# Kernel optimization log

Measured on AMD Instinct MI355X. Metric: run time of the kernel, lower is better.

The kernel has to match this reference:

```python
import jax, jax.numpy as jnp
import numpy as np

N = 1024    # num_points
HID = 1024  # Hamiltonian MLP hidden width


def setup_inputs() -> dict:
    key = jax.random.key(0)
    ks = jax.random.split(key, 6)
    def w(k, shape, fan_in):
        return jax.random.normal(k, shape, dtype=jnp.float32) / np.float32(np.sqrt(fan_in))
    return {
        "x": jax.random.normal(ks[0], (N,), dtype=jnp.float32),
        "q": jax.random.normal(ks[1], (N,), dtype=jnp.float32),
        "p": jax.random.normal(ks[2], (N,), dtype=jnp.float32),
        "W1": w(ks[3], (3 * N, HID), 3 * N),
        "b1": jnp.zeros((HID,), dtype=jnp.float32),
        "W2": w(ks[4], (HID, HID), HID),
        "b2": jnp.zeros((HID,), dtype=jnp.float32),
        "W3": w(ks[5], (HID, 1), HID),
        "b3": jnp.zeros((1,), dtype=jnp.float32),
    }


def _hamiltonian(z, W1, b1, W2, b2, W3, b3):
    # H: R^{3N} -> scalar (matches self.H(cat([x,q,p])).sum())
    h = jnp.tanh(z @ W1 + b1)
    h = jnp.tanh(h @ W2 + b2)
    return jnp.sum(h @ W3 + b3)


def reference(x, q, p, W1, b1, W2, b2, W3, b3):
    n = x.shape[0]

    def grads_qp(x_):
        # (dH/dq, dH/dp) as a function of x, with q,p closed over
        f = lambda q_, p_: _hamiltonian(jnp.concatenate([x_, q_, p_]), W1, b1, W2, b2, W3, b3)
        return jax.grad(f, argnums=(0, 1))(q, p)  # each [n]

    # Diagonal of cross-Hessian blocks via forward-over-reverse, batched over
    # all n basis directions at once (replaces the per-index autograd loop).
    eye = jnp.eye(n, dtype=x.dtype)

    def diag_entry(e_i, i):
        _, (dgq, dgp) = jax.jvp(grads_qp, (x,), (e_i,))
        return dgq[i], dgp[i]  # d2H/(dx_i dq_i), d2H/(dx_i dp_i)

    dH_dq_dx, dH_dp_dx = jax.vmap(diag_entry)(eye, jnp.arange(n))  # each [n]
    return dH_dp_dx, -dH_dq_dx
```

## Files before the change

### kernel.cpp

```cpp
#include <hip/hip_runtime.h>
#include <math.h>

typedef unsigned short u16;
typedef __bf16 bf16x8 __attribute__((ext_vector_type(8)));
typedef float f32x4 __attribute__((ext_vector_type(4)));

__device__ inline u16 bf16_rn(float x) {
    unsigned u = __float_as_uint(x);
    return (u16)((u + 0x7FFFu + ((u >> 16) & 1u)) >> 16);
}
__device__ inline uint2 pack4(u16 a, u16 b, u16 c, u16 d) {
    uint2 r;
    r.x = (unsigned)a | ((unsigned)b << 16);
    r.y = (unsigned)c | ((unsigned)d << 16);
    return r;
}
__device__ inline uint2 pack4f(float a, float b, float c, float d) {
    return pack4(bf16_rn(a), bf16_rn(b), bf16_rn(c), bf16_rn(d));
}
__device__ inline f32x4 mfma16(bf16x8 a, bf16x8 b, f32x4 c) {
    return __builtin_amdgcn_mfma_f32_16x16x32_bf16(a, b, c, 0, 0, 0);
}

__global__ __launch_bounds__(256) void k_pre(const float* __restrict__ x,
                                             const float* __restrict__ q,
                                             const float* __restrict__ p,
                                             const float* __restrict__ W1,
                                             u16* __restrict__ Ah,
                                             float* __restrict__ Upart,
                                             float* __restrict__ out,
                                             float* __restrict__ Vacc) {
    int b = blockIdx.x, t = threadIdx.x;
    if (b < 192) {
        int jc = b;
        int k = (jc & 3) * 256 + t;
        int j0 = (jc >> 2) * 64;
        __shared__ float zs[64];
        if (t < 64) {
            int j = j0 + t;
            zs[t] = (j < 1024) ? x[j] : (j < 2048 ? q[j - 1024] : p[j - 2048]);
        }
        __syncthreads();
        float acc = 0.f;
        if (j0 < 1024) {
#pragma unroll 8
            for (int j = 0; j < 64; ++j) {
                float v = W1[(j0 + j) * 1024 + k];
                Ah[(j0 + j) * 1024 + k] = bf16_rn(v);
                acc += zs[j] * v;
            }
        } else {
#pragma unroll 8
            for (int j = 0; j < 64; ++j) acc += zs[j] * W1[(j0 + j) * 1024 + k];
        }
        Upart[(jc >> 2) * 1024 + k] = acc;
    } else {
        int idx = ((b - 192) * 256 + t) * 4;
        if (idx < 2048) *(float4*)(out + idx) = make_float4(0.f, 0.f, 0.f, 0.f);
        else *(float4*)(Vacc + idx - 2048) = make_float4(0.f, 0.f, 0.f, 0.f);
    }
}

__global__ __launch_bounds__(256) void k_w2v(const float* __restrict__ W2,
                                             const float* __restrict__ b1,
                                             const float* __restrict__ Upart,
                                             float* __restrict__ H1g, float* __restrict__ D1g,
                                             u16* __restrict__ W2h,
                                             u16* __restrict__ WTh,
                                             float* __restrict__ Vacc) {
    __shared__ float T[64][65];
    __shared__ float hs[64], ds[64];
    __shared__ float red[4][64];
    int k0 = blockIdx.y * 64, m0 = blockIdx.x * 64;
    int t = threadIdx.x;
    {
        int lk = t & 63, g = t >> 6;
        float u = 0.f;
#pragma unroll
        for (int c = 0; c < 12; ++c) u += Upart[(g * 12 + c) * 1024 + k0 + lk];
        red[g][lk] = u;
    }
    __syncthreads();
    if (t < 64) {
        float u = red[0][t] + red[1][t] + red[2][t] + red[3][t];
        float h = tanhf(u + b1[k0 + t]);
        hs[t] = h;
        ds[t] = 1.f - h * h;
        if (m0 == 0) { H1g[k0 + t] = h; D1g[k0 + t] = 1.f - h * h; }
    }
    __syncthreads();
    int rr = t >> 4, cc = (t & 15) * 4;
    float4 vp = make_float4(0.f, 0.f, 0.f, 0.f);
#pragma unroll
    for (int j = 0; j < 4; ++j) {
        int r = rr + j * 16;
        float4 v = *(const float4*)(W2 + (k0 + r) * 1024 + m0 + cc);
        T[r][cc + 0] = v.x; T[r][cc + 1] = v.y; T[r][cc + 2] = v.z; T[r][cc + 3] = v.w;
        *(uint2*)&W2h[(k0 + r) * 1024 + m0 + cc] = pack4f(v.x, v.y, v.z, v.w);
        float hk = hs[r];
        vp.x += hk * v.x; vp.y += hk * v.y; vp.z += hk * v.z; vp.w += hk * v.w;
    }
    vp.x += __shfl_xor(vp.x, 16); vp.y += __shfl_xor(vp.y, 16);
    vp.z += __shfl_xor(vp.z, 16); vp.w += __shfl_xor(vp.w, 16);
    vp.x += __shfl_xor(vp.x, 32); vp.y += __shfl_xor(vp.y, 32);
    vp.z += __shfl_xor(vp.z, 32); vp.w += __shfl_xor(vp.w, 32);
    if (((t & 63) >> 4) == 0) {
        atomicAdd(&Vacc[m0 + cc + 0], vp.x);
        atomicAdd(&Vacc[m0 + cc + 1], vp.y);
        atomicAdd(&Vacc[m0 + cc + 2], vp.z);
        atomicAdd(&Vacc[m0 + cc + 3], vp.w);
    }
    __syncthreads();
#pragma unroll
    for (int j = 0; j < 4; ++j) {
        int mrow = rr + j * 16;
        float f0 = T[cc + 0][mrow] * ds[cc + 0];
        float f1 = T[cc + 1][mrow] * ds[cc + 1];
        float f2 = T[cc + 2][mrow] * ds[cc + 2];
        float f3 = T[cc + 3][mrow] * ds[cc + 3];
        *(uint2*)&WTh[(m0 + mrow) * 1024 + k0 + cc] = pack4f(f0, f1, f2, f3);
    }
}

#define LDK 68
__global__ __launch_bounds__(512) void k_gemm1(const u16* __restrict__ Ah,
                                               const u16* __restrict__ Bh,
                                               const float* __restrict__ Vacc,
                                               const float* __restrict__ b2,
                                               const float* __restrict__ W3,
                                               const float* __restrict__ W2,
                                               const float* __restrict__ H1,
                                               const float* __restrict__ D1,
                                               float* __restrict__ Avec,
                                               u16* __restrict__ Sh) {
    __shared__ u16 As[2][64 * LDK];
    __shared__ u16 Bs[2][64 * LDK];
    __shared__ float sv[1024];
    int tid = threadIdx.x;
    if (blockIdx.x == 16) {
        int kbase = blockIdx.y * 64;
#pragma unroll
        for (int j = 0; j < 2; ++j) {
            int m = tid + j * 512;
            float h = tanhf(Vacc[m] + b2[m]);
            sv[m] = (1.f - h * h) * W3[m];
        }
        __syncthreads();
        int g = tid >> 3, sub = tid & 7;
        int k = kbase + g;
        const float* wrow = W2 + k * 1024 + sub * 128;
        const float* svp = sv + sub * 128;
        float acc = 0.f;
#pragma unroll 8
        for (int j = 0; j < 128; ++j) acc += wrow[j] * svp[j];
        acc += __shfl_xor(acc, 1);
        acc += __shfl_xor(acc, 2);
        acc += __shfl_xor(acc, 4);
        if (sub == 0) Avec[k] = -2.f * H1[k] * D1[k] * acc;
        return;
    }
    int lane = tid & 63, wv = tid >> 6;
    int kh = wv >> 2, wy = (wv >> 1) & 1, wx = wv & 1;
    int i0 = blockIdx.y * 64, m0 = blockIdx.x * 64;
    int srow = tid >> 3, sseg = (tid & 7) * 8;
    int ldso = srow * LDK + sseg;
    const u16* ap = Ah + (i0 + srow) * 1024 + sseg;
    const u16* bp = Bh + (m0 + srow) * 1024 + sseg;
    int tx = lane & 15, qy = lane >> 4;
    int koff = kh * 32 + qy * 8;
    int raA[2], rbB[2];
    raA[0] = (wy * 32 + tx) * LDK + koff;
    raA[1] = raA[0] + 16 * LDK;
    rbB[0] = (wx * 32 + tx) * LDK + koff;
    rbB[1] = rbB[0] + 16 * LDK;
    f32x4 acc[2][2];
#pragma unroll
    for (int a = 0; a < 2; ++a)
#pragma unroll
        for (int b = 0; b < 2; ++b) acc[a][b] = (f32x4){0.f, 0.f, 0.f, 0.f};

    uint4 pa1 = *(const uint4*)(ap + 64);
    uint4 pc1 = *(const uint4*)(bp + 64);
    *(uint4*)&As[0][ldso] = *(const uint4*)(ap);
    *(uint4*)&Bs[0][ldso] = *(const uint4*)(bp);

    for (int k0 = 0; k0 < 1024; k0 += 64) {
        int buf = (k0 >> 6) & 1;
        int kn2 = (k0 + 128) & 1023;
        uint4 pa2 = *(const uint4*)(ap + kn2);
        uint4 pc2 = *(const uint4*)(bp + kn2);
        __syncthreads();
        bf16x8 aH0 = *(const bf16x8*)&As[buf][raA[0]];
        bf16x8 aH1 = *(const bf16x8*)&As[buf][raA[1]];
        bf16x8 bH0 = *(const bf16x8*)&Bs[buf][rbB[0]];
        bf16x8 bH1 = *(const bf16x8*)&Bs[buf][rbB[1]];
        acc[0][0] = mfma16(aH0, bH0, acc[0][0]);
        acc[0][1] = mfma16(aH0, bH1, acc[0][1]);
        acc[1][0] = mfma16(aH1, bH0, acc[1][0]);
        acc[1][1] = mfma16(aH1, bH1, acc[1][1]);
        int nb = buf ^ 1;
        *(uint4*)&As[nb][ldso] = pa1;
        *(uint4*)&Bs[nb][ldso] = pc1;
        pa1 = pa2; pc1 = pc2;
    }
    __syncthreads();
    f32x4* mrg = (f32x4*)&As[0][0];
    if (kh == 1) {
#pragma unroll
        for (int si = 0; si < 2; ++si)
#pragma unroll
            for (int sj = 0; sj < 2; ++sj)
                mrg[(((wy * 2 + wx) * 4 + si * 2 + sj) * 4 + qy) * 16 + tx] = acc[si][sj];
    }
    __syncthreads();
    if (kh == 0) {
#pragma unroll
        for (int si = 0; si < 2; ++si)
#pragma unroll
            for (int sj = 0; sj < 2; ++sj) {
                f32x4 o = mrg[(((wy * 2 + wx) * 4 + si * 2 + sj) * 4 + qy) * 16 + tx];
                acc[si][sj][0] += o[0]; acc[si][sj][1] += o[1];
                acc[si][sj][2] += o[2]; acc[si][sj][3] += o[3];
            }
#pragma unroll
        for (int sj = 0; sj < 2; ++sj) {
            int m = m0 + wx * 32 + sj * 16 + tx;
            float hv = tanhf(Vacc[m] + b2[m]);
            float d2 = 1.f - hv * hv;
            float cm = -2.f * hv * d2 * W3[m];
#pragma unroll
            for (int si = 0; si < 2; ++si) {
                int ib = i0 + wy * 32 + si * 16 + qy * 4;
#pragma unroll
                for (int r = 0; r < 4; ++r)
                    Sh[(ib + r) * 1024 + m] = bf16_rn(acc[si][sj][r] * cm);
            }
        }
    }
}

__global__ __launch_bounds__(512) void k_gemm2(const u16* __restrict__ Sh,
                                               const u16* __restrict__ W2h,
                                               const float* __restrict__ W1,
                                               const float* __restrict__ D1,
                                               const float* __restrict__ Avec,
                                               float* __restrict__ out) {
    __shared__ u16 As[2][64 * LDK];
    __shared__ u16 Bs[2][64 * LDK];
    int tid = threadIdx.x, lane = tid & 63, wv = tid >> 6;
    int kh = wv >> 2, wy = (wv >> 1) & 1, wx = wv & 1;
    int i0 = blockIdx.y * 64, k0g = blockIdx.x * 64;
    int srow = tid >> 3, sseg = (tid & 7) * 8;
    int ldso = srow * LDK + sseg;
    const u16* ap = Sh + (i0 + srow) * 1024 + sseg;
    const u16* bp = W2h + (k0g + srow) * 1024 + sseg;
    int tx = lane & 15, qy = lane >> 4;
    int koff = kh * 32 + qy * 8;
    int raA[2], rbB[2];
    raA[0] = (wy * 32 + tx) * LDK + koff;
    raA[1] = raA[0] + 16 * LDK;
    rbB[0] = (wx * 32 + tx) * LDK + koff;
    rbB[1] = rbB[0] + 16 * LDK;
    f32x4 acc[2][2];
#pragma unroll
    for (int a = 0; a < 2; ++a)
#pragma unroll
        for (int b = 0; b < 2; ++b) acc[a][b] = (f32x4){0.f, 0.f, 0.f, 0.f};

    uint4 pa1 = *(const uint4*)(ap + 64);
    uint4 pc1 = *(const uint4*)(bp + 64);
    *(uint4*)&As[0][ldso] = *(const uint4*)(ap);
    *(uint4*)&Bs[0][ldso] = *(const uint4*)(bp);

    for (int m0 = 0; m0 < 1024; m0 += 64) {
        int buf = (m0 >> 6) & 1;
        int mn2 = (m0 + 128) & 1023;
        uint4 pa2 = *(const uint4*)(ap + mn2);
        uint4 pc2 = *(const uint4*)(bp + mn2);
        __syncthreads();
        bf16x8 aH0 = *(const bf16x8*)&As[buf][raA[0]];
        bf16x8 aH1 = *(const bf16x8*)&As[buf][raA[1]];
        bf16x8 bH0 = *(const bf16x8*)&Bs[buf][rbB[0]];
        bf16x8 bH1 = *(const bf16x8*)&Bs[buf][rbB[1]];
        acc[0][0] = mfma16(aH0, bH0, acc[0][0]);
        acc[0][1] = mfma16(aH0, bH1, acc[0][1]);
        acc[1][0] = mfma16(aH1, bH0, acc[1][0]);
        acc[1][1] = mfma16(aH1, bH1, acc[1][1]);
        int nb = buf ^ 1;
        *(uint4*)&As[nb][ldso] = pa1;
        *(uint4*)&Bs[nb][ldso] = pc1;
        pa1 = pa2; pc1 = pc2;
    }
    __syncthreads();
    f32x4* mrg = (f32x4*)&As[0][0];
    if (kh == 1) {
#pragma unroll
        for (int si = 0; si < 2; ++si)
#pragma unroll
            for (int sj = 0; sj < 2; ++sj)
                mrg[(((wy * 2 + wx) * 4 + si * 2 + sj) * 4 + qy) * 16 + tx] = acc[si][sj];
    }
    __syncthreads();
    if (kh == 0) {
#pragma unroll
        for (int si = 0; si < 2; ++si)
#pragma unroll
            for (int sj = 0; sj < 2; ++sj) {
                f32x4 o = mrg[(((wy * 2 + wx) * 4 + si * 2 + sj) * 4 + qy) * 16 + tx];
                acc[si][sj][0] += o[0]; acc[si][sj][1] += o[1];
                acc[si][sj][2] += o[2]; acc[si][sj][3] += o[3];
            }
        int kk[2];
        float d1v[2], avv[2];
#pragma unroll
        for (int sj = 0; sj < 2; ++sj) {
            kk[sj] = k0g + wx * 32 + sj * 16 + tx;
            d1v[sj] = D1[kk[sj]];
            avv[sj] = Avec[kk[sj]];
        }
#pragma unroll
        for (int si = 0; si < 2; ++si) {
            int ib = i0 + wy * 32 + si * 16 + qy * 4;
#pragma unroll
            for (int r = 0; r < 4; ++r) {
                int i = ib + r;
                float pq = 0.f, pp = 0.f;
#pragma unroll
                for (int sj = 0; sj < 2; ++sj) {
                    int k = kk[sj];
                    float dr = avv[sj] * W1[i * 1024 + k] + d1v[sj] * acc[si][sj][r];
                    pq += W1[(1024 + i) * 1024 + k] * dr;
                    pp += W1[(2048 + i) * 1024 + k] * dr;
                }
                for (int o = 1; o < 16; o <<= 1) {
                    pq += __shfl_xor(pq, o);
                    pp += __shfl_xor(pp, o);
                }
                if (tx == 0) {
                    atomicAdd(&out[i], pp);
                    atomicAdd(&out[1024 + i], -pq);
                }
            }
        }
    }
}

extern "C" void kernel_launch(void* const* d_in, const int* in_sizes, int n_in,
                              void* d_out, int out_size, void* d_ws, size_t ws_size,
                              hipStream_t stream) {
    const float* x = (const float*)d_in[0];
    const float* q = (const float*)d_in[1];
    const float* p = (const float*)d_in[2];
    const float* W1 = (const float*)d_in[3];
    const float* b1 = (const float*)d_in[4];
    const float* W2 = (const float*)d_in[5];
    const float* b2 = (const float*)d_in[6];
    const float* W3 = (const float*)d_in[7];
    float* out = (float*)d_out;
    float* ws = (float*)d_ws;
    float* H1 = ws, *D1 = ws + 1024, *Avec = ws + 2048, *Vacc = ws + 3072;
    float* Upart = ws + 4096;
    u16* u0 = (u16*)(ws + 65536);
    u16* Ah = u0;
    u16* WTh = u0 + 1048576;
    u16* W2h = u0 + 2097152;
    u16* Sh = u0 + 3145728;

    k_pre<<<195, 256, 0, stream>>>(x, q, p, W1, Ah, Upart, out, Vacc);
    k_w2v<<<dim3(16, 16), 256, 0, stream>>>(W2, b1, Upart, H1, D1, W2h, WTh, Vacc);
    k_gemm1<<<dim3(17, 16), 512, 0, stream>>>(Ah, WTh, Vacc, b2, W3, W2, H1, D1, Avec, Sh);
    k_gemm2<<<dim3(16, 16), 512, 0, stream>>>(Sh, W2h, W1, D1, Avec, out);
}
```

Before: 119.2 us.

## Fuse four kernels into one cooperative kernel with grid-wide syncs

Replaces the four separate launches (pre, w2v, gemm1, gemm2) with a single cooperative kernel of 256 blocks that uses grid.sync between stages. The Avec matvec that used to run in an extra 17th column of gemm1 blocks is now spread across all blocks after their GEMM tile, and stage work is remapped onto 512-thread blocks. This aims to remove the launch gaps and tail effects between kernels, at the cost of grid-barrier overhead and some threads idling in the stages that only use 256 threads.

Result: slower. 235.0 us (+97.2%).

```diff
diff --git a/kernel.cpp b/kernel.cpp
--- a/kernel.cpp
+++ b/kernel.cpp
@@ -1,5 +1,8 @@
 #include <hip/hip_runtime.h>
+#include <hip/hip_cooperative_groups.h>
 #include <math.h>
+
+namespace cg = cooperative_groups;
 
 typedef unsigned short u16;
 typedef __bf16 bf16x8 __attribute__((ext_vector_type(8)));
@@ -22,123 +25,199 @@
     return __builtin_amdgcn_mfma_f32_16x16x32_bf16(a, b, c, 0, 0, 0);
 }
 
-__global__ __launch_bounds__(256) void k_pre(const float* __restrict__ x,
-                                             const float* __restrict__ q,
-                                             const float* __restrict__ p,
-                                             const float* __restrict__ W1,
-                                             u16* __restrict__ Ah,
-                                             float* __restrict__ Upart,
-                                             float* __restrict__ out,
-                                             float* __restrict__ Vacc) {
-    int b = blockIdx.x, t = threadIdx.x;
-    if (b < 192) {
-        int jc = b;
-        int k = (jc & 3) * 256 + t;
+#define LDK 68
+#define SMEM_BYTES 39040
+
+__global__ __launch_bounds__(512) void k_fused(
+    const float* __restrict__ x, const float* __restrict__ q, const float* __restrict__ p,
+    const float* __restrict__ W1, const float* __restrict__ b1,
+    const float* __restrict__ W2, const float* __restrict__ b2, const float* __restrict__ W3,
+    float* __restrict__ out,
+    float* __restrict__ H1, float* __restrict__ D1, float* __restrict__ Avec,
+    float* __restrict__ Vacc, float* __restrict__ Upart,
+    u16* __restrict__ Ah, u16* __restrict__ WTh, u16* __restrict__ W2h, u16* __restrict__ Sh) {
+    __shared__ __align__(16) char smem[SMEM_BYTES];
+    cg::grid_group grid = cg::this_grid();
+    int tid = threadIdx.x, bid = blockIdx.x;
+
+    if (bid < 96) {
+        float* zs2 = (float*)smem;
+        int half = tid >> 8, t2 = tid & 255;
+        int jc = bid * 2 + half;
+        int k = (jc & 3) * 256 + t2;
         int j0 = (jc >> 2) * 64;
-        __shared__ float zs[64];
-        if (t < 64) {
-            int j = j0 + t;
-            zs[t] = (j < 1024) ? x[j] : (j < 2048 ? q[j - 1024] : p[j - 2048]);
-        }
-        __syncthreads();
+        if (t2 < 64) {
+            int j = j0 + t2;
+            zs2[half * 64 + t2] = (j < 1024) ? x[j] : (j < 2048 ? q[j - 1024] : p[j - 2048]);
+        }
+        __syncthreads();
+        const float* zsl = zs2 + half * 64;
         float acc = 0.f;
         if (j0 < 1024) {
 #pragma unroll 8
             for (int j = 0; j < 64; ++j) {
                 float v = W1[(j0 + j) * 1024 + k];
                 Ah[(j0 + j) * 1024 + k] = bf16_rn(v);
-                acc += zs[j] * v;
+                acc += zsl[j] * v;
             }
         } else {
 #pragma unroll 8
-            for (int j = 0; j < 64; ++j) acc += zs[j] * W1[(j0 + j) * 1024 + k];
+            for (int j = 0; j < 64; ++j) acc += zsl[j] * W1[(j0 + j) * 1024 + k];
         }
         Upart[(jc >> 2) * 1024 + k] = acc;
-    } else {
-        int idx = ((b - 192) * 256 + t) * 4;
-        if (idx < 2048) *(float4*)(out + idx) = make_float4(0.f, 0.f, 0.f, 0.f);
-        else *(float4*)(Vacc + idx - 2048) = make_float4(0.f, 0.f, 0.f, 0.f);
+    } else if (bid == 96) {
+        for (int s = tid; s < 768; s += 512) {
+            int idx = s * 4;
+            if (idx < 2048) *(float4*)(out + idx) = make_float4(0.f, 0.f, 0.f, 0.f);
+            else *(float4*)(Vacc + idx - 2048) = make_float4(0.f, 0.f, 0.f, 0.f);
+        }
     }
-}
-
-__global__ __launch_bounds__(256) void k_w2v(const float* __restrict__ W2,
-                                             const float* __restrict__ b1,
-                                             const float* __restrict__ Upart,
-                                             float* __restrict__ H1g, float* __restrict__ D1g,
-                                             u16* __restrict__ W2h,
-                                             u16* __restrict__ WTh,
-                                             float* __restrict__ Vacc) {
-    __shared__ float T[64][65];
-    __shared__ float hs[64], ds[64];
-    __shared__ float red[4][64];
-    int k0 = blockIdx.y * 64, m0 = blockIdx.x * 64;
-    int t = threadIdx.x;
+    grid.sync();
+
     {
-        int lk = t & 63, g = t >> 6;
-        float u = 0.f;
-#pragma unroll
-        for (int c = 0; c < 12; ++c) u += Upart[(g * 12 + c) * 1024 + k0 + lk];
-        red[g][lk] = u;
+        float(*T)[65] = (float(*)[65])smem;
+        float* red = (float*)(smem + 16640);
+        float* hs = (float*)(smem + 18688);
+        float* ds = (float*)(smem + 18944);
+        int k0 = (bid >> 4) * 64, m0 = (bid & 15) * 64;
+        {
+            int g = tid >> 6, lk = tid & 63;
+            float u = 0.f;
+#pragma unroll
+            for (int c = 0; c < 6; ++c) u += Upart[(g * 6 + c) * 1024 + k0 + lk];
+            red[g * 64 + lk] = u;
+        }
+        __syncthreads();
+        if (tid < 64) {
+            float u = 0.f;
+#pragma unroll
+            for (int g = 0; g < 8; ++g) u += red[g * 64 + tid];
+            float h = tanhf(u + b1[k0 + tid]);
+            hs[tid] = h;
+            ds[tid] = 1.f - h * h;
+            if (m0 == 0) { H1[k0 + tid] = h; D1[k0 + tid] = 1.f - h * h; }
+        }
+        __syncthreads();
+        int t = tid;
+        int rr = (t & 255) >> 4, cc = (t & 15) * 4;
+        if (t < 256) {
+            float4 vp = make_float4(0.f, 0.f, 0.f, 0.f);
+#pragma unroll
+            for (int j = 0; j < 4; ++j) {
+                int r = rr + j * 16;
+                float4 v = *(const float4*)(W2 + (k0 + r) * 1024 + m0 + cc);
+                T[r][cc + 0] = v.x; T[r][cc + 1] = v.y; T[r][cc + 2] = v.z; T[r][cc + 3] = v.w;
+                *(uint2*)&W2h[(k0 + r) * 1024 + m0 + cc] = pack4f(v.x, v.y, v.z, v.w);
+                float hk = hs[r];
+                vp.x += hk * v.x; vp.y += hk * v.y; vp.z += hk * v.z; vp.w += hk * v.w;
+            }
+            vp.x += __shfl_xor(vp.x, 16); vp.y += __shfl_xor(vp.y, 16);
+            vp.z += __shfl_xor(vp.z, 16); vp.w += __shfl_xor(vp.w, 16);
+            vp.x += __shfl_xor(vp.x, 32); vp.y += __shfl_xor(vp.y, 32);
+            vp.z += __shfl_xor(vp.z, 32); vp.w += __shfl_xor(vp.w, 32);
+            if (((t & 63) >> 4) == 0) {
+                atomicAdd(&Vacc[m0 + cc + 0], vp.x);
+                atomicAdd(&Vacc[m0 + cc + 1], vp.y);
+                atomicAdd(&Vacc[m0 + cc + 2], vp.z);
+                atomicAdd(&Vacc[m0 + cc + 3], vp.w);
+            }
+        }
+        __syncthreads();
+        if (t < 256) {
+#pragma unroll
+            for (int j = 0; j < 4; ++j) {
+                int mrow = rr + j * 16;
+                float f0 = T[cc + 0][mrow] * ds[cc + 0];
+                float f1 = T[cc + 1][mrow] * ds[cc + 1];
+                float f2 = T[cc + 2][mrow] * ds[cc + 2];
+                float f3 = T[cc + 3][mrow] * ds[cc + 3];
+                *(uint2*)&WTh[(m0 + mrow) * 1024 + k0 + cc] = pack4f(f0, f1, f2, f3);
+            }
+        }
     }
-    __syncthreads();
-    if (t < 64) {
-        float u = red[0][t] + red[1][t] + red[2][t] + red[3][t];
-        float h = tanhf(u + b1[k0 + t]);
-        hs[t] = h;
-        ds[t] = 1.f - h * h;
-        if (m0 == 0) { H1g[k0 + t] = h; D1g[k0 + t] = 1.f - h * h; }
-    }
-    __syncthreads();
-    int rr = t >> 4, cc = (t & 15) * 4;
-    float4 vp = make_float4(0.f, 0.f, 0.f, 0.f);
-#pragma unroll
-    for (int j = 0; j < 4; ++j) {
-        int r = rr + j * 16;
-        float4 v = *(const float4*)(W2 + (k0 + r) * 1024 + m0 + cc);
-        T[r][cc + 0] = v.x; T[r][cc + 1] = v.y; T[r][cc + 2] = v.z; T[r][cc + 3] = v.w;
-        *(uint2*)&W2h[(k0 + r) * 1024 + m0 + cc] = pack4f(v.x, v.y, v.z, v.w);
-        float hk = hs[r];
-        vp.x += hk * v.x; vp.y += hk * v.y; vp.z += hk * v.z; vp.w += hk * v.w;
-    }
-    vp.x += __shfl_xor(vp.x, 16); vp.y += __shfl_xor(vp.y, 16);
-    vp.z += __shfl_xor(vp.z, 16); vp.w += __shfl_xor(vp.w, 16);
-    vp.x += __shfl_xor(vp.x, 32); vp.y += __shfl_xor(vp.y, 32);
-    vp.z += __shfl_xor(vp.z, 32); vp.w += __shfl_xor(vp.w, 32);
-    if (((t & 63) >> 4) == 0) {
-        atomicAdd(&Vacc[m0 + cc + 0], vp.x);
-        atomicAdd(&Vacc[m0 + cc + 1], vp.y);
-        atomicAdd(&Vacc[m0 + cc + 2], vp.z);
-        atomicAdd(&Vacc[m0 + cc + 3], vp.w);
-    }
-    __syncthreads();
-#pragma unroll
-    for (int j = 0; j < 4; ++j) {
-        int mrow = rr + j * 16;
-        float f0 = T[cc + 0][mrow] * ds[cc + 0];
-        float f1 = T[cc + 1][mrow] * ds[cc + 1];
-        float f2 = T[cc + 2][mrow] * ds[cc + 2];
-        float f3 = T[cc + 3][mrow] * ds[cc + 3];
-        *(uint2*)&WTh[(m0 + mrow) * 1024 + k0 + cc] = pack4f(f0, f1, f2, f3);
-    }
-}
-
-#define LDK 68
-__global__ __launch_bounds__(512) void k_gemm1(const u16* __restrict__ Ah,
-                                               const u16* __restrict__ Bh,
-                                               const float* __restrict__ Vacc,
-                                               const float* __restrict__ b2,
-                                               const float* __restrict__ W3,
-                                               const float* __restrict__ W2,
-                                               const float* __restrict__ H1,
-                                               const float* __restrict__ D1,
-                                               float* __restrict__ Avec,
-                                               u16* __restrict__ Sh) {
-    __shared__ u16 As[2][64 * LDK];
-    __shared__ u16 Bs[2][64 * LDK];
-    __shared__ float sv[1024];
-    int tid = threadIdx.x;
-    if (blockIdx.x == 16) {
-        int kbase = blockIdx.y * 64;
+    grid.sync();
+
+    {
+        u16* As = (u16*)smem;
+        u16* Bs = (u16*)(smem + 17408);
+        float* sv = (float*)(smem + 34816);
+        float* redA = (float*)(smem + 38912);
+        int lane = tid & 63, wv = tid >> 6;
+        int kh = wv >> 2, wy = (wv >> 1) & 1, wx = wv & 1;
+        int i0 = (bid >> 4) * 64, m0 = (bid & 15) * 64;
+        int srow = tid >> 3, sseg = (tid & 7) * 8;
+        int ldso = srow * LDK + sseg;
+        const u16* ap = Ah + (i0 + srow) * 1024 + sseg;
+        const u16* bp = WTh + (m0 + srow) * 1024 + sseg;
+        int tx = lane & 15, qy = lane >> 4;
+        int koff = kh * 32 + qy * 8;
+        int raA0 = (wy * 32 + tx) * LDK + koff, raA1 = raA0 + 16 * LDK;
+        int rbB0 = (wx * 32 + tx) * LDK + koff, rbB1 = rbB0 + 16 * LDK;
+        f32x4 acc[2][2];
+#pragma unroll
+        for (int a = 0; a < 2; ++a)
+#pragma unroll
+            for (int b = 0; b < 2; ++b) acc[a][b] = (f32x4){0.f, 0.f, 0.f, 0.f};
+
+        uint4 pa1 = *(const uint4*)(ap + 64);
+        uint4 pc1 = *(const uint4*)(bp + 64);
+        *(uint4*)&As[ldso] = *(const uint4*)(ap);
+        *(uint4*)&Bs[ldso] = *(const uint4*)(bp);
+
+        for (int k0 = 0; k0 < 1024; k0 += 64) {
+            int buf = ((k0 >> 6) & 1) * 4352;
+            int kn2 = (k0 + 128) & 1023;
+            uint4 pa2 = *(const uint4*)(ap + kn2);
+            uint4 pc2 = *(const uint4*)(bp + kn2);
+            __syncthreads();
+            bf16x8 aH0 = *(const bf16x8*)&As[buf + raA0];
+            bf16x8 aH1 = *(const bf16x8*)&As[buf + raA1];
+            bf16x8 bH0 = *(const bf16x8*)&Bs[buf + rbB0];
+            bf16x8 bH1 = *(const bf16x8*)&Bs[buf + rbB1];
+            acc[0][0] = mfma16(aH0, bH0, acc[0][0]);
+            acc[0][1] = mfma16(aH0, bH1, acc[0][1]);
+            acc[1][0] = mfma16(aH1, bH0, acc[1][0]);
+            acc[1][1] = mfma16(aH1, bH1, acc[1][1]);
+            int nb = buf ^ 4352;
+            *(uint4*)&As[nb + ldso] = pa1;
+            *(uint4*)&Bs[nb + ldso] = pc1;
+            pa1 = pa2; pc1 = pc2;
+        }
+        __syncthreads();
+        f32x4* mrg = (f32x4*)As;
+        if (kh == 1) {
+#pragma unroll
+            for (int si = 0; si < 2; ++si)
+#pragma unroll
+                for (int sj = 0; sj < 2; ++sj)
+                    mrg[(((wy * 2 + wx) * 4 + si * 2 + sj) * 4 + qy) * 16 + tx] = acc[si][sj];
+        }
+        __syncthreads();
+        if (kh == 0) {
+#pragma unroll
+            for (int si = 0; si < 2; ++si)
+#pragma unroll
+                for (int sj = 0; sj < 2; ++sj) {
+                    f32x4 o = mrg[(((wy * 2 + wx) * 4 + si * 2 + sj) * 4 + qy) * 16 + tx];
+                    acc[si][sj][0] += o[0]; acc[si][sj][1] += o[1];
+                    acc[si][sj][2] += o[2]; acc[si][sj][3] += o[3];
+                }
+#pragma unroll
+            for (int sj = 0; sj < 2; ++sj) {
+                int m = m0 + wx * 32 + sj * 16 + tx;
+                float hv = tanhf(Vacc[m] + b2[m]);
+                float d2 = 1.f - hv * hv;
+                float cm = -2.f * hv * d2 * W3[m];
+#pragma unroll
+                for (int si = 0; si < 2; ++si) {
+                    int ib = i0 + wy * 32 + si * 16 + qy * 4;
+#pragma unroll
+                    for (int r = 0; r < 4; ++r)
+                        Sh[(ib + r) * 1024 + m] = bf16_rn(acc[si][sj][r] * cm);
+                }
+            }
+        }
+        __syncthreads();
 #pragma unroll
         for (int j = 0; j < 2; ++j) {
             int m = tid + j * 512;
@@ -146,199 +225,119 @@
             sv[m] = (1.f - h * h) * W3[m];
         }
         __syncthreads();
-        int g = tid >> 3, sub = tid & 7;
-        int k = kbase + g;
-        const float* wrow = W2 + k * 1024 + sub * 128;
-        const float* svp = sv + sub * 128;
-        float acc = 0.f;
-#pragma unroll 8
-        for (int j = 0; j < 128; ++j) acc += wrow[j] * svp[j];
-        acc += __shfl_xor(acc, 1);
-        acc += __shfl_xor(acc, 2);
-        acc += __shfl_xor(acc, 4);
-        if (sub == 0) Avec[k] = -2.f * H1[k] * D1[k] * acc;
-        return;
+        {
+            int kA = bid * 4 + (wv >> 1);
+            int off = (wv & 1) * 512 + lane * 8;
+            const float* wr = W2 + kA * 1024 + off;
+            const float* svp = sv + off;
+            float a = 0.f;
+#pragma unroll
+            for (int j = 0; j < 8; ++j) a += wr[j] * svp[j];
+#pragma unroll
+            for (int o = 1; o < 64; o <<= 1) a += __shfl_xor(a, o);
+            if (lane == 0) redA[wv] = a;
+        }
+        __syncthreads();
+        if (tid < 4) {
+            int kA = bid * 4 + tid;
+            Avec[kA] = -2.f * H1[kA] * D1[kA] * (redA[tid * 2] + redA[tid * 2 + 1]);
+        }
     }
-    int lane = tid & 63, wv = tid >> 6;
-    int kh = wv >> 2, wy = (wv >> 1) & 1, wx = wv & 1;
-    int i0 = blockIdx.y * 64, m0 = blockIdx.x * 64;
-    int srow = tid >> 3, sseg = (tid & 7) * 8;
-    int ldso = srow * LDK + sseg;
-    const u16* ap = Ah + (i0 + srow) * 1024 + sseg;
-    const u16* bp = Bh + (m0 + srow) * 1024 + sseg;
-    int tx = lane & 15, qy = lane >> 4;
-    int koff = kh * 32 + qy * 8;
-    int raA[2], rbB[2];
-    raA[0] = (wy * 32 + tx) * LDK + koff;
-    raA[1] = raA[0] + 16 * LDK;
-    rbB[0] = (wx * 32 + tx) * LDK + koff;
-    rbB[1] = rbB[0] + 16 * LDK;
-    f32x4 acc[2][2];
-#pragma unroll
-    for (int a = 0; a < 2; ++a)
-#pragma unroll
-        for (int b = 0; b < 2; ++b) acc[a][b] = (f32x4){0.f, 0.f, 0.f, 0.f};
-
-    uint4 pa1 = *(const uint4*)(ap + 64);
-    uint4 pc1 = *(const uint4*)(bp + 64);
-    *(uint4*)&As[0][ldso] = *(const uint4*)(ap);
-    *(uint4*)&Bs[0][ldso] = *(const uint4*)(bp);
-
-    for (int k0 = 0; k0 < 1024; k0 += 64) {
-        int buf = (k0 >> 6) & 1;
-        int kn2 = (k0 + 128) & 1023;
-        uint4 pa2 = *(const uint4*)(ap + kn2);
-        uint4 pc2 = *(const uint4*)(bp + kn2);
-        __syncthreads();
-        bf16x8 aH0 = *(const bf16x8*)&As[buf][raA[0]];
-        bf16x8 aH1 = *(const bf16x8*)&As[buf][raA[1]];
-        bf16x8 bH0 = *(const bf16x8*)&Bs[buf][rbB[0]];
-        bf16x8 bH1 = *(const bf16x8*)&Bs[buf][rbB[1]];
-        acc[0][0] = mfma16(aH0, bH0, acc[0][0]);
-        acc[0][1] = mfma16(aH0, bH1, acc[0][1]);
-        acc[1][0] = mfma16(aH1, bH0, acc[1][0]);
-        acc[1][1] = mfma16(aH1, bH1, acc[1][1]);
-        int nb = buf ^ 1;
-        *(uint4*)&As[nb][ldso] = pa1;
-        *(uint4*)&Bs[nb][ldso] = pc1;
-        pa1 = pa2; pc1 = pc2;
-    }
-    __syncthreads();
-    f32x4* mrg = (f32x4*)&As[0][0];
-    if (kh == 1) {
-#pragma unroll
-        for (int si = 0; si < 2; ++si)
-#pragma unroll
-            for (int sj = 0; sj < 2; ++sj)
-                mrg[(((wy * 2 + wx) * 4 + si * 2 + sj) * 4 + qy) * 16 + tx] = acc[si][sj];
-    }
-    __syncthreads();
-    if (kh == 0) {
-#pragma unroll
-        for (int si = 0; si < 2; ++si)
+    grid.sync();
+
+    {
+        u16* As = (u16*)smem;
+        u16* Bs = (u16*)(smem + 17408);
+        int lane = tid & 63, wv = tid >> 6;
+        int kh = wv >> 2, wy = (wv >> 1) & 1, wx = wv & 1;
+        int i0 = (bid >> 4) * 64, k0g = (bid & 15) * 64;
+        int srow = tid >> 3, sseg = (tid & 7) * 8;
+        int ldso = srow * LDK + sseg;
+        const u16* ap = Sh + (i0 + srow) * 1024 + sseg;
+        const u16* bp = W2h + (k0g + srow) * 1024 + sseg;
+        int tx = lane & 15, qy = lane >> 4;
+        int koff = kh * 32 + qy * 8;
+        int raA0 = (wy * 32 + tx) * LDK + koff, raA1 = raA0 + 16 * LDK;
+        int rbB0 = (wx * 32 + tx) * LDK + koff, rbB1 = rbB0 + 16 * LDK;
+        f32x4 acc[2][2];
+#pragma unroll
+        for (int a = 0; a < 2; ++a)
+#pragma unroll
+            for (int b = 0; b < 2; ++b) acc[a][b] = (f32x4){0.f, 0.f, 0.f, 0.f};
+
+        uint4 pa1 = *(const uint4*)(ap + 64);
+        uint4 pc1 = *(const uint4*)(bp + 64);
+        *(uint4*)&As[ldso] = *(const uint4*)(ap);
+        *(uint4*)&Bs[ldso] = *(const uint4*)(bp);
+
+        for (int m0 = 0; m0 < 1024; m0 += 64) {
+            int buf = ((m0 >> 6) & 1) * 4352;
+            int mn2 = (m0 + 128) & 1023;
+            uint4 pa2 = *(const uint4*)(ap + mn2);
+            uint4 pc2 = *(const uint4*)(bp + mn2);
+            __syncthreads();
+            bf16x8 aH0 = *(const bf16x8*)&As[buf + raA0];
+            bf16x8 aH1 = *(const bf16x8*)&As[buf + raA1];
+            bf16x8 bH0 = *(const bf16x8*)&Bs[buf + rbB0];
+            bf16x8 bH1 = *(const bf16x8*)&Bs[buf + rbB1];
+            acc[0][0] = mfma16(aH0, bH0, acc[0][0]);
+            acc[0][1] = mfma16(aH0, bH1, acc[0][1]);
+            acc[1][0] = mfma16(aH1, bH0, acc[1][0]);
+            acc[1][1] = mfma16(aH1, bH1, acc[1][1]);
+            int nb = buf ^ 4352;
+            *(uint4*)&As[nb + ldso] = pa1;
+            *(uint4*)&Bs[nb + ldso] = pc1;
+            pa1 = pa2; pc1 = pc2;
+        }
+        __syncthreads();
+        f32x4* mrg = (f32x4*)As;
+        if (kh == 1) {
+#pragma unroll
+            for (int si = 0; si < 2; ++si)
+#pragma unroll
+                for (int sj = 0; sj < 2; ++sj)
+                    mrg[(((wy * 2 + wx) * 4 + si * 2 + sj) * 4 + qy) * 16 + tx] = acc[si][sj];
+        }
+        __syncthreads();
+        if (kh == 0) {
+#pragma unroll
+            for (int si = 0; si < 2; ++si)
+#pragma unroll
+                for (int sj = 0; sj < 2; ++sj) {
+                    f32x4 o = mrg[(((wy * 2 + wx) * 4 + si * 2 + sj) * 4 + qy) * 16 + tx];
+                    acc[si][sj][0] += o[0]; acc[si][sj][1] += o[1];
+                    acc[si][sj][2] += o[2]; acc[si][sj][3] += o[3];
+                }
+            int kk[2];
+            float d1v[2], avv[2];
 #pragma unroll
             for (int sj = 0; sj < 2; ++sj) {
-                f32x4 o = mrg[(((wy * 2 + wx) * 4 + si * 2 + sj) * 4 + qy) * 16 + tx];
-                acc[si][sj][0] += o[0]; acc[si][sj][1] += o[1];
-                acc[si][sj][2] += o[2]; acc[si][sj][3] += o[3];
-            }
-#pragma unroll
-        for (int sj = 0; sj < 2; ++sj) {
-            int m = m0 + wx * 32 + sj * 16 + tx;
-            float hv = tanhf(Vacc[m] + b2[m]);
-            float d2 = 1.f - hv * hv;
-            float cm = -2.f * hv * d2 * W3[m];
+                kk[sj] = k0g + wx * 32 + sj * 16 + tx;
+                d1v[sj] = D1[kk[sj]];
+                avv[sj] = Avec[kk[sj]];
+            }
 #pragma unroll
             for (int si = 0; si < 2; ++si) {
                 int ib = i0 + wy * 32 + si * 16 + qy * 4;
 #pragma unroll
-                for (int r = 0; r < 4; ++r)
-                    Sh[(ib + r) * 1024 + m] = bf16_rn(acc[si][sj][r] * cm);
-            }
-        }
-    }
-}
-
-__global__ __launch_bounds__(512) void k_gemm2(const u16* __restrict__ Sh,
-                                               const u16* __restrict__ W2h,
-                                               const float* __restrict__ W1,
-                                               const float* __restrict__ D1,
-                                               const float* __restrict__ Avec,
-                                               float* __restrict__ out) {
-    __shared__ u16 As[2][64 * LDK];
-    __shared__ u16 Bs[2][64 * LDK];
-    int tid = threadIdx.x, lane = tid & 63, wv = tid >> 6;
-    int kh = wv >> 2, wy = (wv >> 1) & 1, wx = wv & 1;
-    int i0 = blockIdx.y * 64, k0g = blockIdx.x * 64;
-    int srow = tid >> 3, sseg = (tid & 7) * 8;
-    int ldso = srow * LDK + sseg;
-    const u16* ap = Sh + (i0 + srow) * 1024 + sseg;
-    const u16* bp = W2h + (k0g + srow) * 1024 + sseg;
-    int tx = lane & 15, qy = lane >> 4;
-    int koff = kh * 32 + qy * 8;
-    int raA[2], rbB[2];
-    raA[0] = (wy * 32 + tx) * LDK + koff;
-    raA[1] = raA[0] + 16 * LDK;
-    rbB[0] = (wx * 32 + tx) * LDK + koff;
-    rbB[1] = rbB[0] + 16 * LDK;
-    f32x4 acc[2][2];
-#pragma unroll
-    for (int a = 0; a < 2; ++a)
-#pragma unroll
-        for (int b = 0; b < 2; ++b) acc[a][b] = (f32x4){0.f, 0.f, 0.f, 0.f};
-
-    uint4 pa1 = *(const uint4*)(ap + 64);
-    uint4 pc1 = *(const uint4*)(bp + 64);
-    *(uint4*)&As[0][ldso] = *(const uint4*)(ap);
-    *(uint4*)&Bs[0][ldso] = *(const uint4*)(bp);
-
-    for (int m0 = 0; m0 < 1024; m0 += 64) {
-        int buf = (m0 >> 6) & 1;
-        int mn2 = (m0 + 128) & 1023;
-        uint4 pa2 = *(const uint4*)(ap + mn2);
-        uint4 pc2 = *(const uint4*)(bp + mn2);
-        __syncthreads();
-        bf16x8 aH0 = *(const bf16x8*)&As[buf][raA[0]];
-        bf16x8 aH1 = *(const bf16x8*)&As[buf][raA[1]];
-        bf16x8 bH0 = *(const bf16x8*)&Bs[buf][rbB[0]];
-        bf16x8 bH1 = *(const bf16x8*)&Bs[buf][rbB[1]];
-        acc[0][0] = mfma16(aH0, bH0, acc[0][0]);
-        acc[0][1] = mfma16(aH0, bH1, acc[0][1]);
-        acc[1][0] = mfma16(aH1, bH0, acc[1][0]);
-        acc[1][1] = mfma16(aH1, bH1, acc[1][1]);
-        int nb = buf ^ 1;
-        *(uint4*)&As[nb][ldso] = pa1;
-        *(uint4*)&Bs[nb][ldso] = pc1;
-        pa1 = pa2; pc1 = pc2;
-    }
-    __syncthreads();
-    f32x4* mrg = (f32x4*)&As[0][0];
-    if (kh == 1) {
-#pragma unroll
-        for (int si = 0; si < 2; ++si)
-#pragma unroll
-            for (int sj = 0; sj < 2; ++sj)
-                mrg[(((wy * 2 + wx) * 4 + si * 2 + sj) * 4 + qy) * 16 + tx] = acc[si][sj];
-    }
-    __syncthreads();
-    if (kh == 0) {
-#pragma unroll
-        for (int si = 0; si < 2; ++si)
-#pragma unroll
-            for (int sj = 0; sj < 2; ++sj) {
-                f32x4 o = mrg[(((wy * 2 + wx) * 4 + si * 2 + sj) * 4 + qy) * 16 + tx];
-                acc[si][sj][0] += o[0]; acc[si][sj][1] += o[1];
-                acc[si][sj][2] += o[2]; acc[si][sj][3] += o[3];
-            }
-        int kk[2];
-        float d1v[2], avv[2];
-#pragma unroll
-        for (int sj = 0; sj < 2; ++sj) {
-            kk[sj] = k0g + wx * 32 + sj * 16 + tx;
-            d1v[sj] = D1[kk[sj]];
-            avv[sj] = Avec[kk[sj]];
-        }
-#pragma unroll
-        for (int si = 0; si < 2; ++si) {
-            int ib = i0 + wy * 32 + si * 16 + qy * 4;
-#pragma unroll
-            for (int r = 0; r < 4; ++r) {
-                int i = ib + r;
-                float pq = 0.f, pp = 0.f;
-#pragma unroll
-                for (int sj = 0; sj < 2; ++sj) {
-                    int k = kk[sj];
-                    float dr = avv[sj] * W1[i * 1024 + k] + d1v[sj] * acc[si][sj][r];
-                    pq += W1[(1024 + i) * 1024 + k] * dr;
-                    pp += W1[(2048 + i) * 1024 + k] * dr;
-                }
-                for (int o = 1; o < 16; o <<= 1) {
-                    pq += __shfl_xor(pq, o);
-                    pp += __shfl_xor(pp, o);
-                }
-                if (tx == 0) {
-                    atomicAdd(&out[i], pp);
-                    atomicAdd(&out[1024 + i], -pq);
+                for (int r = 0; r < 4; ++r) {
+                    int i = ib + r;
+                    float pq = 0.f, pp = 0.f;
+#pragma unroll
+                    for (int sj = 0; sj < 2; ++sj) {
+                        int k = kk[sj];
+                        float dr = avv[sj] * W1[i * 1024 + k] + d1v[sj] * acc[si][sj][r];
+                        pq += W1[(1024 + i) * 1024 + k] * dr;
+                        pp += W1[(2048 + i) * 1024 + k] * dr;
+                    }
+                    for (int o = 1; o < 16; o <<= 1) {
+                        pq += __shfl_xor(pq, o);
+                        pp += __shfl_xor(pp, o);
+                    }
+                    if (tx == 0) {
+                        atomicAdd(&out[i], pp);
+                        atomicAdd(&out[1024 + i], -pq);
+                    }
                 }
             }
         }
@@ -366,8 +365,7 @@
     u16* W2h = u0 + 2097152;
     u16* Sh = u0 + 3145728;
 
-    k_pre<<<195, 256, 0, stream>>>(x, q, p, W1, Ah, Upart, out, Vacc);
-    k_w2v<<<dim3(16, 16), 256, 0, stream>>>(W2, b1, Upart, H1, D1, W2h, WTh, Vacc);
-    k_gemm1<<<dim3(17, 16), 512, 0, stream>>>(Ah, WTh, Vacc, b2, W3, W2, H1, D1, Avec, Sh);
-    k_gemm2<<<dim3(16, 16), 512, 0, stream>>>(Sh, W2h, W1, D1, Avec, out);
-}
+    void* args[] = {&x, &q, &p, &W1, &b1, &W2, &b2, &W3, &out,
+                    &H1, &D1, &Avec, &Vacc, &Upart, &Ah, &WTh, &W2h, &Sh};
+    hipLaunchCooperativeKernel((const void*)k_fused, dim3(256), dim3(512), args, 0, stream);
+}
```
